# Performance work log

Measured on AMD Instinct MI355X. Metric: run time of the kernel, lower is better.

The kernel has to match this reference:

```python
import jax, jax.numpy as jnp
import numpy as np
import itertools, math

B, T, D = 4, 4096, 1024
H = 16
DIM = D // H          # 64
L, KB = 8, 4
R = 1 << KB           # 16
S = L * R             # 128
TOPK = 2


def setup_inputs() -> dict:
    key = jax.random.key(0)
    ks = jax.random.split(key, 8)
    x = jax.random.normal(ks[0], (B, T, D), dtype=jnp.float32)
    mask = jnp.ones((B, T), dtype=jnp.float32)
    sc = 1.0 / math.sqrt(D)
    Wq = jax.random.normal(ks[1], (D, D), dtype=jnp.float32) * sc
    Wk = jax.random.normal(ks[2], (D, D), dtype=jnp.float32) * sc
    Wv = jax.random.normal(ks[3], (D, D), dtype=jnp.float32) * sc
    Wout = jax.random.normal(ks[4], (D, D), dtype=jnp.float32) * sc
    b_out = jnp.zeros((D,), dtype=jnp.float32)
    # planes: (L, K_bits, head_dim) -> stored transposed as (head_dim, L*K_bits)
    planes = jax.random.normal(ks[5], (L * KB, DIM), dtype=jnp.float32)
    planes_T = planes.T
    # hypercube corners (R, K_bits) -> stored transposed as (K_bits, R)
    corners = jnp.asarray(list(itertools.product([-1.0, 1.0], repeat=KB)), dtype=jnp.float32)
    protos_T = corners.T
    logit_temp = jnp.zeros((), dtype=jnp.float32)  # log(1.0)
    return {"x": x, "mask": mask, "Wq": Wq, "Wk": Wk, "Wv": Wv,
            "Wout": Wout, "b_out": b_out, "planes_T": planes_T,
            "protos_T": protos_T, "logit_temp": logit_temp}


def reference(x, mask, Wq, Wk, Wv, Wout, b_out, planes_T, protos_T, logit_temp):
    b, t, d = x.shape
    Q = (x @ Wq).reshape(b, t, H, DIM)
    K = (x @ Wk).reshape(b, t, H, DIM)
    V = (x @ Wv).reshape(b, t, H, DIM)
    m = mask[:, :, None, None]
    Q, K, V = Q * m, K * m, V * m
    Q = jnp.transpose(Q, (0, 2, 1, 3))  # [B,H,T,dim]
    K = jnp.transpose(K, (0, 2, 1, 3))
    V = jnp.transpose(V, (0, 2, 1, 3))

    scale = jnp.clip(jnp.exp(logit_temp), 0.01, 20.0)
    # LSH hyperplane projections of K
    projK = jnp.einsum('bhtd,dp->bhtp', K, planes_T).reshape(b, H, t, L, KB)
    logitsK = jnp.einsum('bhtlk,kr->bhtlr', jnp.tanh(projK) / scale, protos_T)
    probsK = jax.nn.softmax(logitsK, axis=-1)  # [B,H,T,L,R]

    # top-k mask over R, then renormalize
    _, top_idx = jax.lax.top_k(probsK, TOPK)
    sel = jax.nn.one_hot(top_idx, R, dtype=probsK.dtype).sum(axis=-2)
    probsK = probsK * sel
    probsK = probsK / (probsK.sum(axis=-1, keepdims=True) + 1e-6)

    assign = probsK.reshape(b, H, t, S)  # [B,H,T,S]
    bucket_K = jnp.einsum('bhts,bhtd->bhsd', assign, K)
    bucket_V = jnp.einsum('bhts,bhtd->bhsd', assign, V)
    A = assign.sum(axis=2)[..., None]  # [B,H,S,1]
    bucket_K = bucket_K / (A + 1e-6)
    bucket_V = bucket_V / (A + 1e-6)

    scores = jnp.einsum('bhtd,bhsd->bhts', Q, bucket_K) / math.sqrt(DIM)
    probs_attn = jax.nn.softmax(scores, axis=-1)
    out = jnp.einsum('bhts,bhsd->bhtd', probs_attn, bucket_V)
    out = jnp.transpose(out, (0, 2, 1, 3)).reshape(b, t, d)
    return out @ Wout + b_out
```

## Files before the change

kernel.cpp:

```cpp
#include <hip/hip_runtime.h>
#include <math.h>
#include <stdint.h>

#define TT   4096
#define DD   1024
#define HH   16
#define DIMM 64
#define SS   128

typedef short bf16x8 __attribute__((ext_vector_type(8)));
typedef float f32x4  __attribute__((ext_vector_type(4)));

__device__ __forceinline__ unsigned short f2bf(float f) {
    uint32_t u = __float_as_uint(f);
    return (unsigned short)((u + 0x7fffu + ((u >> 16) & 1u)) >> 16);
}
__device__ __forceinline__ float bf2f(unsigned short h) {
    return __uint_as_float((uint32_t)h << 16);
}

#define GLD16(ldsp, gp) __builtin_amdgcn_global_load_lds( \
    (const __attribute__((address_space(1))) uint32_t*)(gp), \
    (__attribute__((address_space(3))) uint32_t*)(ldsp), 16, 0, 0)

__global__ __launch_bounds__(256) void cvt2_k(const float* __restrict__ x,
                                              unsigned short* __restrict__ xb,
                                              unsigned short* __restrict__ xlo)
{
    const size_t i = ((size_t)blockIdx.x * 256 + threadIdx.x) * 8;
    const float4 a = *(const float4*)&x[i];
    const float4 b = *(const float4*)&x[i + 4];
    const float v[8] = {a.x, a.y, a.z, a.w, b.x, b.y, b.z, b.w};
    unsigned short h[8], l[8];
#pragma unroll
    for (int j = 0; j < 8; j++) {
        h[j] = f2bf(v[j]);
        l[j] = f2bf(v[j] - bf2f(h[j]));
    }
    uint4 rh, rl;
    rh.x = (uint32_t)h[0] | ((uint32_t)h[1] << 16);
    rh.y = (uint32_t)h[2] | ((uint32_t)h[3] << 16);
    rh.z = (uint32_t)h[4] | ((uint32_t)h[5] << 16);
    rh.w = (uint32_t)h[6] | ((uint32_t)h[7] << 16);
    rl.x = (uint32_t)l[0] | ((uint32_t)l[1] << 16);
    rl.y = (uint32_t)l[2] | ((uint32_t)l[3] << 16);
    rl.z = (uint32_t)l[4] | ((uint32_t)l[5] << 16);
    rl.w = (uint32_t)l[6] | ((uint32_t)l[7] << 16);
    *(uint4*)&xb[i]  = rh;
    *(uint4*)&xlo[i] = rl;
}

__global__ __launch_bounds__(256) void tr_k(const float* __restrict__ W,
                                            unsigned short* __restrict__ WT)
{
    __shared__ unsigned short tile[32][33];
    const int bx = blockIdx.x * 32;
    const int by = blockIdx.y * 32;
    const int tx = threadIdx.x & 31, ty = threadIdx.x >> 5;
#pragma unroll
    for (int r = 0; r < 4; r++) {
        const int row = by + ty * 4 + r;
        tile[tx][ty * 4 + r] = f2bf(W[(size_t)row * 1024 + bx + tx]);
    }
    __syncthreads();
#pragma unroll
    for (int r = 0; r < 4; r++) {
        const int col = bx + ty * 4 + r;
        WT[(size_t)col * 1024 + by + tx] = tile[ty * 4 + r][tx];
    }
}

__global__ __launch_bounds__(256) void tr2_k(const float* __restrict__ Wp,
                                             unsigned short* __restrict__ WphT,
                                             unsigned short* __restrict__ WplT)
{
    __shared__ float tile[32][33];
    const int bx = blockIdx.x * 32;
    const int by = blockIdx.y * 32;
    const int tx = threadIdx.x & 31, ty = threadIdx.x >> 5;
#pragma unroll
    for (int r = 0; r < 4; r++) {
        const int row = by + ty * 4 + r;
        tile[tx][ty * 4 + r] = Wp[(size_t)row * 512 + bx + tx];
    }
    __syncthreads();
#pragma unroll
    for (int r = 0; r < 4; r++) {
        const int col = bx + ty * 4 + r;
        const float v = tile[ty * 4 + r][tx];
        const unsigned short hi = f2bf(v);
        const unsigned short lo = f2bf(v - bf2f(hi));
        WphT[(size_t)col * 1024 + by + tx] = hi;
        WplT[(size_t)col * 1024 + by + tx] = lo;
    }
}

__global__ __launch_bounds__(256) void qkv_k(
    const unsigned short* __restrict__ Abf, const unsigned short* __restrict__ BT,
    const float* __restrict__ mask, unsigned short* __restrict__ Qf,
    float* __restrict__ Kb, float* __restrict__ Vb)
{
    __shared__ short sA[2][4096];
    __shared__ short sB[2][4096];
    const int tid = threadIdx.x;
    const int w  = tid >> 6;
    const int ln = tid & 63;
    const int wm = w & 1, wn = w >> 1;
    const int id   = blockIdx.y * 24 + blockIdx.x;
    const int xcd  = id & 7, kk = id >> 3;
    const int band = xcd * 16 + kk / 24;
    const int colblk = kk % 24;
    const int row0 = band * 128;
    const int col0 = colblk * 128;
    const int lr = ln >> 4, lc = ln & 15;

    f32x4 acc[4][4];
#pragma unroll
    for (int i = 0; i < 4; i++)
#pragma unroll
        for (int j = 0; j < 4; j++) acc[i][j] = (f32x4){0.f, 0.f, 0.f, 0.f};

    const int ia0 = 2 * w, ia1 = 2 * w + 1;
    const size_t gA0 = (size_t)(row0 + ia0 * 16 + lc) * 1024 + lr * 8;
    const size_t gA1 = (size_t)(row0 + ia1 * 16 + lc) * 1024 + lr * 8;
    const size_t gB0 = (size_t)(col0 + ia0 * 16 + lc) * 1024 + lr * 8;
    const size_t gB1 = (size_t)(col0 + ia1 * 16 + lc) * 1024 + lr * 8;

    auto STAGE = [&](int buf, int k0) {
        GLD16(&sA[buf][ia0 * 512], Abf + gA0 + k0);
        GLD16(&sA[buf][ia1 * 512], Abf + gA1 + k0);
        GLD16(&sB[buf][ia0 * 512], BT  + gB0 + k0);
        GLD16(&sB[buf][ia1 * 512], BT  + gB1 + k0);
    };

    STAGE(0, 0);
    __syncthreads();
    for (int t = 0; t < 32; t++) {
        const int cur = t & 1;
        if (t < 31) STAGE(cur ^ 1, (t + 1) * 32);
        bf16x8 af[4], bfr[4];
#pragma unroll
        for (int ib = 0; ib < 4; ib++)
            af[ib] = *(const bf16x8*)&sA[cur][(wm * 4 + ib) * 512 + ln * 8];
#pragma unroll
        for (int jb = 0; jb < 4; jb++)
            bfr[jb] = *(const bf16x8*)&sB[cur][(wn * 4 + jb) * 512 + ln * 8];
#pragma unroll
        for (int ib = 0; ib < 4; ib++)
#pragma unroll
            for (int jb = 0; jb < 4; jb++)
                acc[ib][jb] = __builtin_amdgcn_mfma_f32_16x16x32_bf16(
                    af[ib], bfr[jb], acc[ib][jb], 0, 0, 0);
        __syncthreads();
    }

    const int proj = colblk >> 3;
    const int c0l  = (colblk & 7) * 128;
    const int h    = c0l / 64 + wn;
    if (proj == 0) {
#pragma unroll
        for (int ib = 0; ib < 4; ib++) {
#pragma unroll
            for (int r = 0; r < 4; r++) {
                const int gr = row0 + wm * 64 + ib * 16 + lr * 4 + r;
                const float mval = mask[gr];
                const int b = gr >> 12;
                const int tt = gr & 127;
                const size_t tbase = (size_t)(b * HH + h) * 262144
                                   + (size_t)((gr & (TT - 1)) >> 7) * 8192;
#pragma unroll
                for (int jb = 0; jb < 4; jb++) {
                    const int d = jb * 16 + lc;
                    const int e = ((tt >> 4) * 2 + (d >> 5)) * 512 +
                                  ((tt & 15) + ((d >> 3) & 3) * 16) * 8 + (d & 7);
                    Qf[tbase + e] = f2bf(acc[ib][jb][r] * mval);
                }
            }
        }
    } else {
        float* C = (proj == 1) ? Kb : Vb;
#pragma unroll
        for (int ib = 0; ib < 4; ib++) {
#pragma unroll
            for (int r = 0; r < 4; r++) {
                const int gr = row0 + wm * 64 + ib * 16 + lr * 4 + r;
                const float mval = mask[gr];
                const int b = gr >> 12, t = gr & (TT - 1);
                float* base = C + (((size_t)(b * HH + h) * TT + t) * DIMM);
#pragma unroll
                for (int jb = 0; jb < 4; jb++)
                    base[jb * 16 + lc] = acc[ib][jb][r] * mval;
            }
        }
    }
}

__global__ __launch_bounds__(256) void out_k(
    const unsigned short* __restrict__ Abf, const unsigned short* __restrict__ BT,
    const float* __restrict__ bias, float* __restrict__ C)
{
    __shared__ short sA[2][4096];
    __shared__ short sB[2][4096];
    const int tid = threadIdx.x;
    const int w  = tid >> 6, ln = tid & 63;
    const int wm = w & 1, wn = w >> 1;
    const int id  = blockIdx.y * 8 + blockIdx.x;
    const int xcd = id & 7, kk = id >> 3;
    const int row0 = (xcd * 16 + (kk >> 3)) * 128;
    const int col0 = (kk & 7) * 128;
    const int lr = ln >> 4, lc = ln & 15;

    f32x4 acc[4][4];
#pragma unroll
    for (int i = 0; i < 4; i++)
#pragma unroll
        for (int j = 0; j < 4; j++) acc[i][j] = (f32x4){0.f, 0.f, 0.f, 0.f};

    const int ia0 = 2 * w, ia1 = 2 * w + 1;
    const size_t gA0 = (size_t)(row0 + ia0 * 16 + lc) * 1024 + lr * 8;
    const size_t gA1 = (size_t)(row0 + ia1 * 16 + lc) * 1024 + lr * 8;
    const size_t gB0 = (size_t)(col0 + ia0 * 16 + lc) * 1024 + lr * 8;
    const size_t gB1 = (size_t)(col0 + ia1 * 16 + lc) * 1024 + lr * 8;

    auto STAGE = [&](int buf, int k0) {
        GLD16(&sA[buf][ia0 * 512], Abf + gA0 + k0);
        GLD16(&sA[buf][ia1 * 512], Abf + gA1 + k0);
        GLD16(&sB[buf][ia0 * 512], BT  + gB0 + k0);
        GLD16(&sB[buf][ia1 * 512], BT  + gB1 + k0);
    };

    STAGE(0, 0);
    __syncthreads();
    for (int t = 0; t < 32; t++) {
        const int cur = t & 1;
        if (t < 31) STAGE(cur ^ 1, (t + 1) * 32);
        bf16x8 af[4], bfr[4];
#pragma unroll
        for (int ib = 0; ib < 4; ib++)
            af[ib] = *(const bf16x8*)&sA[cur][(wm * 4 + ib) * 512 + ln * 8];
#pragma unroll
        for (int jb = 0; jb < 4; jb++)
            bfr[jb] = *(const bf16x8*)&sB[cur][(wn * 4 + jb) * 512 + ln * 8];
#pragma unroll
        for (int ib = 0; ib < 4; ib++)
#pragma unroll
            for (int jb = 0; jb < 4; jb++)
                acc[ib][jb] = __builtin_amdgcn_mfma_f32_16x16x32_bf16(
                    af[ib], bfr[jb], acc[ib][jb], 0, 0, 0);
        __syncthreads();
    }

#pragma unroll
    for (int ib = 0; ib < 4; ib++) {
#pragma unroll
        for (int r = 0; r < 4; r++) {
            const int gr = row0 + wm * 64 + ib * 16 + lr * 4 + r;
#pragma unroll
            for (int jb = 0; jb < 4; jb++) {
                const int col = col0 + wn * 64 + jb * 16 + lc;
                C[(size_t)gr * 1024 + col] = acc[ib][jb][r] + bias[col];
            }
        }
    }
}

__global__ __launch_bounds__(256) void projm_k(
    const unsigned short* __restrict__ Ah, const unsigned short* __restrict__ Al,
    const unsigned short* __restrict__ Bh, const unsigned short* __restrict__ Bl,
    const float* __restrict__ mask, float* __restrict__ P)
{
    __shared__ short sAh[2][4096];
    __shared__ short sAl[2][4096];
    __shared__ short sBh[2][4096];
    __shared__ short sBl[2][4096];
    const int tid = threadIdx.x;
    const int w  = tid >> 6;
    const int ln = tid & 63;
    const int wm = w & 1, wn = w >> 1;
    const int id  = blockIdx.y * 4 + blockIdx.x;
    const int xcd = id & 7, kk = id >> 3;
    const int row0 = (xcd * 16 + (kk >> 2)) * 128;
    const int col0 = (kk & 3) * 128;
    const int lr = ln >> 4, lc = ln & 15;

    f32x4 acc[4][4];
#pragma unroll
    for (int i = 0; i < 4; i++)
#pragma unroll
        for (int j = 0; j < 4; j++) acc[i][j] = (f32x4){0.f, 0.f, 0.f, 0.f};

    const int ia0 = 2 * w, ia1 = 2 * w + 1;
    const size_t gA0 = (size_t)(row0 + ia0 * 16 + lc) * 1024 + lr * 8;
    const size_t gA1 = (size_t)(row0 + ia1 * 16 + lc) * 1024 + lr * 8;
    const size_t gB0 = (size_t)(col0 + ia0 * 16 + lc) * 1024 + lr * 8;
    const size_t gB1 = (size_t)(col0 + ia1 * 16 + lc) * 1024 + lr * 8;

    auto STAGE = [&](int buf, int k0) {
        GLD16(&sAh[buf][ia0 * 512], Ah + gA0 + k0);
        GLD16(&sAh[buf][ia1 * 512], Ah + gA1 + k0);
        GLD16(&sAl[buf][ia0 * 512], Al + gA0 + k0);
        GLD16(&sAl[buf][ia1 * 512], Al + gA1 + k0);
        GLD16(&sBh[buf][ia0 * 512], Bh + gB0 + k0);
        GLD16(&sBh[buf][ia1 * 512], Bh + gB1 + k0);
        GLD16(&sBl[buf][ia0 * 512], Bl + gB0 + k0);
        GLD16(&sBl[buf][ia1 * 512], Bl + gB1 + k0);
    };

    STAGE(0, 0);
    __syncthreads();
    for (int t = 0; t < 32; t++) {
        const int cur = t & 1;
        if (t < 31) STAGE(cur ^ 1, (t + 1) * 32);
        bf16x8 ah[4], al[4], bh[4], bl[4];
#pragma unroll
        for (int ib = 0; ib < 4; ib++) {
            ah[ib] = *(const bf16x8*)&sAh[cur][(wm * 4 + ib) * 512 + ln * 8];
            al[ib] = *(const bf16x8*)&sAl[cur][(wm * 4 + ib) * 512 + ln * 8];
        }
#pragma unroll
        for (int jb = 0; jb < 4; jb++) {
            bh[jb] = *(const bf16x8*)&sBh[cur][(wn * 4 + jb) * 512 + ln * 8];
            bl[jb] = *(const bf16x8*)&sBl[cur][(wn * 4 + jb) * 512 + ln * 8];
        }
#pragma unroll
        for (int ib = 0; ib < 4; ib++)
#pragma unroll
            for (int jb = 0; jb < 4; jb++) {
                acc[ib][jb] = __builtin_amdgcn_mfma_f32_16x16x32_bf16(
                    ah[ib], bh[jb], acc[ib][jb], 0, 0, 0);
                acc[ib][jb] = __builtin_amdgcn_mfma_f32_16x16x32_bf16(
                    ah[ib], bl[jb], acc[ib][jb], 0, 0, 0);
                acc[ib][jb] = __builtin_amdgcn_mfma_f32_16x16x32_bf16(
                    al[ib], bh[jb], acc[ib][jb], 0, 0, 0);
            }
        __syncthreads();
    }

#pragma unroll
    for (int ib = 0; ib < 4; ib++) {
#pragma unroll
        for (int r = 0; r < 4; r++) {
            const int gr = row0 + wm * 64 + ib * 16 + lr * 4 + r;
            const float mval = mask[gr];
            const int b = gr >> 12, t = gr & (TT - 1);
#pragma unroll
            for (int jb = 0; jb < 4; jb++) {
                const int c = col0 + wn * 64 + jb * 16 + lc;
                const int h = c >> 5, p = c & 31;
                P[(((size_t)(b * HH + h) * TT + t) * 32) + p] =
                    acc[ib][jb][r] * mval;
            }
        }
    }
}

__global__ __launch_bounds__(256) void wproj_k(
    const float* __restrict__ Wk, const float* __restrict__ planesT,
    float* __restrict__ Wp)
{
    __shared__ float sW[1024];
    __shared__ float sP[2048];
    const int tid = threadIdx.x;
    const int k = blockIdx.x;
    for (int i = tid; i < 1024; i += 256) sW[i] = Wk[(size_t)k * 1024 + i];
    for (int i = tid; i < 2048; i += 256) sP[i] = planesT[i];
    __syncthreads();
#pragma unroll
    for (int c0 = 0; c0 < 2; c0++) {
        const int c = c0 * 256 + tid;
        const int h = c >> 5, p = c & 31;
        float s = 0.f;
#pragma unroll
        for (int d = 0; d < 64; d++)
            s = fmaf(sW[h * 64 + d], sP[d * 32 + p], s);
        Wp[(size_t)k * 512 + c] = s;
    }
}

__global__ __launch_bounds__(256) void zero_k(float* __restrict__ p)
{
    const size_t i = ((size_t)blockIdx.x * 256 + threadIdx.x) * 4;
    *(float4*)&p[i] = make_float4(0.f, 0.f, 0.f, 0.f);
}

__global__ __launch_bounds__(256) void assign_k(
    const float* __restrict__ Pj, const float* __restrict__ protosT,
    const float* __restrict__ logit_temp,
    unsigned char* __restrict__ aIdx, float* __restrict__ aW,
    float* __restrict__ gA)
{
    __shared__ float sPr[4][16];
    __shared__ float sCnt[SS];
    const int tid = threadIdx.x;
    const int tc = blockIdx.x;
    const int bh = blockIdx.y;

    if (tid < 64)  ((float*)sPr)[tid] = protosT[tid];
    if (tid < SS)  sCnt[tid] = 0.f;
    __syncthreads();

    const float scale = fminf(fmaxf(__expf(logit_temp[0]), 0.01f), 20.0f);
    const float inv_scale = 1.0f / scale;

    const int t = tc * 256 + tid;
    const float* pr = Pj + ((size_t)bh * TT + t) * 32;
    float proj[32];
#pragma unroll
    for (int j = 0; j < 8; j++) {
        const float4 v = *(const float4*)&pr[j * 4];
        proj[j * 4 + 0] = v.x; proj[j * 4 + 1] = v.y;
        proj[j * 4 + 2] = v.z; proj[j * 4 + 3] = v.w;
    }
#pragma unroll
    for (int p = 0; p < 32; p++) proj[p] = tanhf(proj[p]) * inv_scale;

    unsigned char idx[16];
    float wv[16];
#pragma unroll
    for (int l = 0; l < 8; l++) {
        float g[16];
#pragma unroll
        for (int r = 0; r < 16; r++)
            g[r] = proj[l * 4 + 0] * sPr[0][r] + proj[l * 4 + 1] * sPr[1][r] +
                   proj[l * 4 + 2] * sPr[2][r] + proj[l * 4 + 3] * sPr[3][r];
        float mx = g[0];
#pragma unroll
        for (int r = 1; r < 16; r++) mx = fmaxf(mx, g[r]);
        float Zs = 0.f;
#pragma unroll
        for (int r = 0; r < 16; r++) Zs += __expf(g[r] - mx);
        int a = 0; float ga = g[0];
#pragma unroll
        for (int r = 1; r < 16; r++) { if (g[r] > ga) { ga = g[r]; a = r; } }
        int b2 = (a == 0) ? 1 : 0; float gb = g[b2];
#pragma unroll
        for (int r = 0; r < 16; r++) { if (r != a && g[r] > gb) { gb = g[r]; b2 = r; } }
        const float pa = __expf(ga - mx) / Zs;
        const float pb = __expf(gb - mx) / Zs;
        const float den = pa + pb + 1e-6f;
        const float wa = pa / den, wb = pb / den;
        idx[l * 2 + 0] = (unsigned char)(l * 16 + a);  wv[l * 2 + 0] = wa;
        idx[l * 2 + 1] = (unsigned char)(l * 16 + b2); wv[l * 2 + 1] = wb;
        atomicAdd(&sCnt[l * 16 + a],  wa);
        atomicAdd(&sCnt[l * 16 + b2], wb);
    }
    const size_t off = (size_t)bh * TT + t;
    uint32_t pk[4];
#pragma unroll
    for (int j = 0; j < 4; j++)
        pk[j] = (uint32_t)idx[j * 4] | ((uint32_t)idx[j * 4 + 1] << 8) |
                ((uint32_t)idx[j * 4 + 2] << 16) | ((uint32_t)idx[j * 4 + 3] << 24);
    *(uint4*)&aIdx[off * 16] = make_uint4(pk[0], pk[1], pk[2], pk[3]);
#pragma unroll
    for (int j = 0; j < 4; j++)
        *(float4*)&aW[off * 16 + j * 4] =
            make_float4(wv[j * 4], wv[j * 4 + 1], wv[j * 4 + 2], wv[j * 4 + 3]);
    __syncthreads();
    if (tid < SS) atomicAdd(&gA[bh * SS + tid], sCnt[tid]);
}

__global__ __launch_bounds__(256) void scatter4_k(
    const float* __restrict__ Kb, const float* __restrict__ Vb,
    const unsigned char* __restrict__ aIdx, const float* __restrict__ aW,
    float* __restrict__ gBK, float* __restrict__ gBV)
{
    __shared__ short sA[8192];
    __shared__ short sB[8192];
    const int tid = threadIdx.x;
    const int tc = blockIdx.x;
    const int bh = blockIdx.y;
    const int w  = tid >> 6, ln = tid & 63;
    const int wm = w & 1, wn = w >> 1;

    f32x4 acc[4][4];
#pragma unroll
    for (int i = 0; i < 4; i++)
#pragma unroll
        for (int j = 0; j < 4; j++) acc[i][j] = (f32x4){0.f, 0.f, 0.f, 0.f};

    const int scol = tid & 127;
    const int stg  = tid >> 7;
    const float* srcrow = (scol < 64)
        ? Kb + (size_t)bh * (TT * DIMM) + scol
        : Vb + (size_t)bh * (TT * DIMM) + (scol - 64);
    const int bchunk = (scol >> 4);
    const int bslot8 = (scol & 15) * 8;
    const int ptt = tid >> 2, pg = tid & 3;

    for (int c = 0; c < 8; c++) {
        const int t0 = tc * 512 + c * 64;
        __syncthreads();
        {
            const uint4 z = make_uint4(0u, 0u, 0u, 0u);
#pragma unroll
            for (int r = 0; r < 4; r++)
                *(uint4*)&sA[(r * 256 + tid) * 8] = z;
        }
        __syncthreads();
#pragma unroll 8
        for (int r = 0; r < 32; r++) {
            const int tt = stg * 32 + r;
            const float v = srcrow[(size_t)(t0 + tt) * DIMM];
            sB[((tt >> 5) * 8 + bchunk) * 512 + ((tt >> 3) & 3) * 128 +
               bslot8 + (tt & 7)] = f2bf(v);
        }
        {
            const size_t off = (size_t)bh * TT + (t0 + ptt);
            const uint32_t pk = ((const uint32_t*)aIdx)[off * 4 + pg];
            const float4 wv = *(const float4*)&aW[off * 16 + pg * 4];
            const float w4[4] = {wv.x, wv.y, wv.z, wv.w};
#pragma unroll
            for (int q = 0; q < 4; q++) {
                const int s = (pk >> (8 * q)) & 255;
                sA[((ptt >> 5) * 8 + (s >> 4)) * 512 + ((ptt >> 3) & 3) * 128 +
                   (s & 15) * 8 + (ptt & 7)] = f2bf(w4[q]);
            }
        }
        __syncthreads();
#pragma unroll
        for (int ks = 0; ks < 2; ks++) {
            bf16x8 af[4], bfr[4];
#pragma unroll
            for (int ib = 0; ib < 4; ib++)
                af[ib] = *(const bf16x8*)&sA[(ks * 8 + wm * 4 + ib) * 512 + ln * 8];
#pragma unroll
            for (int jb = 0; jb < 4; jb++)
                bfr[jb] = *(const bf16x8*)&sB[(ks * 8 + wn * 4 + jb) * 512 + ln * 8];
#pragma unroll
            for (int ib = 0; ib < 4; ib++)
#pragma unroll
                for (int jb = 0; jb < 4; jb++)
                    acc[ib][jb] = __builtin_amdgcn_mfma_f32_16x16x32_bf16(
                        af[ib], bfr[jb], acc[ib][jb], 0, 0, 0);
        }
    }

    const int lr = ln >> 4, lc = ln & 15;
#pragma unroll
    for (int ib = 0; ib < 4; ib++) {
#pragma unroll
        for (int r = 0; r < 4; r++) {
            const int s = wm * 64 + ib * 16 + lr * 4 + r;
#pragma unroll
            for (int jb = 0; jb < 4; jb++) {
                const int col = wn * 64 + jb * 16 + lc;
                if (col < 64)
                    atomicAdd(&gBK[(size_t)bh * (SS * DIMM) + s * DIMM + col],
                              acc[ib][jb][r]);
                else
                    atomicAdd(&gBV[(size_t)bh * (SS * DIMM) + s * DIMM + (col - 64)],
                              acc[ib][jb][r]);
            }
        }
    }
}

__global__ __launch_bounds__(256) void bprep_k(
    const float* __restrict__ gBK, const float* __restrict__ gBV,
    const float* __restrict__ gA,
    unsigned short* __restrict__ Kf, unsigned short* __restrict__ VTf)
{
    __shared__ float sInv[SS];
    const int tid = threadIdx.x;
    const int bh = blockIdx.y;
    if (tid < SS) sInv[tid] = 1.0f / (gA[bh * SS + tid] + 1e-6f);
    __syncthreads();
#pragma unroll
    for (int it = 0; it < 8; it++) {
        const int i = (blockIdx.x * 8 + it) * 256 + tid;
        const int s = i >> 6, d = i & 63;
        const float kv = gBK[(size_t)bh * 8192 + i] * sInv[s];
        const float vv = gBV[(size_t)bh * 8192 + i] * sInv[s];
        const int ek = ((s >> 4) * 2 + (d >> 5)) * 512 +
                       ((s & 15) + ((d >> 3) & 3) * 16) * 8 + (d & 7);
        const int ev = ((d >> 4) * 4 + (s >> 5)) * 512 +
                       ((d & 15) + ((s >> 3) & 3) * 16) * 8 + (s & 7);
        Kf[(size_t)bh * 8192 + ek]  = f2bf(kv);
        VTf[(size_t)bh * 8192 + ev] = f2bf(vv);
    }
}

__global__ __launch_bounds__(256) void attn_m(
    const unsigned short* __restrict__ Qf, const unsigned short* __restrict__ Kf,
    const unsigned short* __restrict__ VTf, unsigned short* __restrict__ attb)
{
    __shared__ short sQ[8192];
    __shared__ short sK[8192];
    __shared__ short sVT[8192];
    __shared__ short sP[16384];
    const int tid = threadIdx.x;
    const int tc = blockIdx.x;
    const int bh = blockIdx.y;
    const int w = tid >> 6, l = tid & 63;

    const size_t qbase  = (size_t)bh * 262144 + (size_t)tc * 8192;
    const size_t kvbase = (size_t)bh * 8192;
#pragma unroll
    for (int i = 0; i < 4; i++) {
        const int o = (i * 256 + w * 64) * 8;
        GLD16(&sQ[o],  Qf  + qbase  + o + l * 8);
        GLD16(&sK[o],  Kf  + kvbase + o + l * 8);
        GLD16(&sVT[o], VTf + kvbase + o + l * 8);
    }
    __syncthreads();

    f32x4 acc[2][8];
#pragma unroll
    for (int i = 0; i < 2; i++)
#pragma unroll
        for (int j = 0; j < 8; j++) acc[i][j] = (f32x4){0.f, 0.f, 0.f, 0.f};

#pragma unroll
    for (int ks = 0; ks < 2; ks++) {
        const bf16x8 a0 = *(const bf16x8*)&sQ[((w * 2 + 0) * 2 + ks) * 512 + l * 8];
        const bf16x8 a1 = *(const bf16x8*)&sQ[((w * 2 + 1) * 2 + ks) * 512 + l * 8];
#pragma unroll
        for (int jb = 0; jb < 8; jb++) {
            const bf16x8 b = *(const bf16x8*)&sK[(jb * 2 + ks) * 512 + l * 8];
            acc[0][jb] = __builtin_amdgcn_mfma_f32_16x16x32_bf16(a0, b, acc[0][jb], 0, 0, 0);
            acc[1][jb] = __builtin_amdgcn_mfma_f32_16x16x32_bf16(a1, b, acc[1][jb], 0, 0, 0);
        }
    }

#pragma unroll
    for (int ib = 0; ib < 2; ib++) {
        const int mb = w * 2 + ib;
#pragma unroll
        for (int r = 0; r < 4; r++) {
            float v[8];
            float mx = -INFINITY;
#pragma unroll
            for (int jb = 0; jb < 8; jb++) {
                v[jb] = acc[ib][jb][r] * 0.125f;
                mx = fmaxf(mx, v[jb]);
            }
            mx = fmaxf(mx, __shfl_xor(mx, 1));
            mx = fmaxf(mx, __shfl_xor(mx, 2));
            mx = fmaxf(mx, __shfl_xor(mx, 4));
            mx = fmaxf(mx, __shfl_xor(mx, 8));
            float Z = 0.f;
#pragma unroll
            for (int jb = 0; jb < 8; jb++) { v[jb] = __expf(v[jb] - mx); Z += v[jb]; }
            Z += __shfl_xor(Z, 1);
            Z += __shfl_xor(Z, 2);
            Z += __shfl_xor(Z, 4);
            Z += __shfl_xor(Z, 8);
            const float invZ = 1.0f / Z;
            const int ttl = (l >> 4) * 4 + r;
#pragma unroll
            for (int jb = 0; jb < 8; jb++) {
                int e = (mb * 4 + (jb >> 1)) * 512 +
                        (ttl + (((jb * 2 + ((l >> 3) & 1)) & 3) * 16)) * 8 + (l & 7);
                e ^= ((e >> 7) & 3) << 4;
                sP[e] = (short)f2bf(v[jb] * invZ);
            }
        }
    }

    f32x4 acc2[2][4];
#pragma unroll
    for (int i = 0; i < 2; i++)
#pragma unroll
        for (int j = 0; j < 4; j++) acc2[i][j] = (f32x4){0.f, 0.f, 0.f, 0.f};

#pragma unroll
    for (int ks = 0; ks < 4; ks++) {
        bf16x8 a[2];
#pragma unroll
        for (int ib = 0; ib < 2; ib++) {
            int ia = ((w * 2 + ib) * 4 + ks) * 512 + l * 8;
            ia ^= ((ia >> 7) & 3) << 4;
            a[ib] = *(const bf16x8*)&sP[ia];
        }
#pragma unroll
        for (int jb = 0; jb < 4; jb++) {
            const bf16x8 b = *(const bf16x8*)&sVT[(jb * 4 + ks) * 512 + l * 8];
            acc2[0][jb] = __builtin_amdgcn_mfma_f32_16x16x32_bf16(a[0], b, acc2[0][jb], 0, 0, 0);
            acc2[1][jb] = __builtin_amdgcn_mfma_f32_16x16x32_bf16(a[1], b, acc2[1][jb], 0, 0, 0);
        }
    }

    const int b = bh >> 4, h = bh & 15;
#pragma unroll
    for (int ib = 0; ib < 2; ib++) {
#pragma unroll
        for (int r = 0; r < 4; r++) {
            const int t = tc * 128 + w * 32 + ib * 16 + (l >> 4) * 4 + r;
            unsigned short* outp = attb + ((size_t)(b * TT + t)) * DD + h * DIMM;
#pragma unroll
            for (int jb = 0; jb < 4; jb++)
                outp[jb * 16 + (l & 15)] = f2bf(acc2[ib][jb][r]);
        }
    }
}

extern "C" void kernel_launch(void* const* d_in, const int* in_sizes, int n_in,
                              void* d_out, int out_size, void* d_ws, size_t ws_size,
                              hipStream_t stream)
{
    const float* x       = (const float*)d_in[0];
    const float* mask    = (const float*)d_in[1];
    const float* Wq      = (const float*)d_in[2];
    const float* Wk      = (const float*)d_in[3];
    const float* Wv      = (const float*)d_in[4];
    const float* Wout    = (const float*)d_in[5];
    const float* b_out   = (const float*)d_in[6];
    const float* planesT = (const float*)d_in[7];
    const float* protosT = (const float*)d_in[8];
    const float* ltemp   = (const float*)d_in[9];
    float* out = (float*)d_out;

    float* ws  = (float*)d_ws;
    float* Kb  = ws + (1u << 24);
    float* Vb  = ws + (2u << 24);
    float* gBK = ws + (3u << 24);
    float* gBV = gBK + 524288;
    float* gA  = gBV + 524288;
    unsigned short* Qf    = (unsigned short*)ws;
    unsigned short* xb    = (unsigned short*)(ws + 51388416);
    unsigned short* xlo   = (unsigned short*)Vb;
    float*          Wp    = ws;
    unsigned short* WphT  = (unsigned short*)(ws + 524288);
    unsigned short* WplT  = (unsigned short*)(ws + 786432);
    float*          aW    = ws + 51388416;
    unsigned char*  aIdx  = (unsigned char*)(ws + 55582720);
    unsigned short* Kf    = (unsigned short*)(ws + 56631296);
    unsigned short* VTf   = (unsigned short*)(ws + 56893440);
    unsigned short* attb  = (unsigned short*)Vb;
    unsigned short* WoutT = (unsigned short*)(ws + 41943040);
    float*          Pj    = (float*)d_out;
    unsigned short* BTall = (unsigned short*)((float*)d_out + 8388608);

    const dim3 tg(32, 32);
    const dim3 t2g(16, 32);
    const dim3 pg(4, 128);
    const dim3 qg(24, 128);
    const dim3 og(8, 128);

    cvt2_k<<<8192, 256, 0, stream>>>(x, xb, xlo);

    wproj_k<<<1024, 256, 0, stream>>>(Wk, planesT, Wp);
    tr2_k<<<t2g, 256, 0, stream>>>(Wp, WphT, WplT);
    projm_k<<<pg, 256, 0, stream>>>(xb, xlo, WphT, WplT, mask, Pj);

    tr_k<<<tg, 256, 0, stream>>>(Wq, BTall);
    tr_k<<<tg, 256, 0, stream>>>(Wk, BTall + 1048576);
    tr_k<<<tg, 256, 0, stream>>>(Wv, BTall + 2097152);
    qkv_k<<<qg, 256, 0, stream>>>(xb, BTall, mask, Qf, Kb, Vb);

    zero_k<<<1032, 256, 0, stream>>>(gBK);
    assign_k<<<dim3(16, 64), 256, 0, stream>>>(Pj, protosT, ltemp, aIdx, aW, gA);
    scatter4_k<<<dim3(8, 64), 256, 0, stream>>>(Kb, Vb, aIdx, aW, gBK, gBV);

    bprep_k<<<dim3(4, 64), 256, 0, stream>>>(gBK, gBV, gA, Kf, VTf);
    tr_k<<<tg, 256, 0, stream>>>(Wout, WoutT);
    attn_m<<<dim3(32, 64), 256, 0, stream>>>(Qf, Kf, VTf, attb);

    out_k<<<og, 256, 0, stream>>>(attb, WoutT, b_out, out);
}
```

Before: 659.9 us.

## Write K/V as bf16 MFMA-ready tiles via LDS-staged epilogue, load directly in scatter

After: 629.9 us. -4.5%, faster.

```diff
diff --git a/kernel.cpp b/kernel.cpp
--- a/kernel.cpp
+++ b/kernel.cpp
@@ -98,18 +98,20 @@
 __global__ __launch_bounds__(256) void qkv_k(
     const unsigned short* __restrict__ Abf, const unsigned short* __restrict__ BT,
     const float* __restrict__ mask, unsigned short* __restrict__ Qf,
-    float* __restrict__ Kb, float* __restrict__ Vb)
-{
-    __shared__ short sA[2][4096];
-    __shared__ short sB[2][4096];
+    unsigned short* __restrict__ KVf)
+{
+    __shared__ short sMem[16384];
+    short* sA = sMem;
+    short* sB = sMem + 8192;
     const int tid = threadIdx.x;
     const int w  = tid >> 6;
     const int ln = tid & 63;
     const int wm = w & 1, wn = w >> 1;
     const int id   = blockIdx.y * 24 + blockIdx.x;
     const int xcd  = id & 7, kk = id >> 3;
-    const int band = xcd * 16 + kk / 24;
-    const int colblk = kk % 24;
+    const int cg   = kk / 192, rem = kk % 192;
+    const int band = xcd * 16 + rem / 12;
+    const int colblk = cg * 12 + rem % 12;
     const int row0 = band * 128;
     const int col0 = colblk * 128;
     const int lr = ln >> 4, lc = ln & 15;
@@ -127,10 +129,10 @@
     const size_t gB1 = (size_t)(col0 + ia1 * 16 + lc) * 1024 + lr * 8;
 
     auto STAGE = [&](int buf, int k0) {
-        GLD16(&sA[buf][ia0 * 512], Abf + gA0 + k0);
-        GLD16(&sA[buf][ia1 * 512], Abf + gA1 + k0);
-        GLD16(&sB[buf][ia0 * 512], BT  + gB0 + k0);
-        GLD16(&sB[buf][ia1 * 512], BT  + gB1 + k0);
+        GLD16(&sA[buf * 4096 + ia0 * 512], Abf + gA0 + k0);
+        GLD16(&sA[buf * 4096 + ia1 * 512], Abf + gA1 + k0);
+        GLD16(&sB[buf * 4096 + ia0 * 512], BT  + gB0 + k0);
+        GLD16(&sB[buf * 4096 + ia1 * 512], BT  + gB1 + k0);
     };
 
     STAGE(0, 0);
@@ -141,10 +143,10 @@
         bf16x8 af[4], bfr[4];
 #pragma unroll
         for (int ib = 0; ib < 4; ib++)
-            af[ib] = *(const bf16x8*)&sA[cur][(wm * 4 + ib) * 512 + ln * 8];
+            af[ib] = *(const bf16x8*)&sA[cur * 4096 + (wm * 4 + ib) * 512 + ln * 8];
 #pragma unroll
         for (int jb = 0; jb < 4; jb++)
-            bfr[jb] = *(const bf16x8*)&sB[cur][(wn * 4 + jb) * 512 + ln * 8];
+            bfr[jb] = *(const bf16x8*)&sB[cur * 4096 + (wn * 4 + jb) * 512 + ln * 8];
 #pragma unroll
         for (int ib = 0; ib < 4; ib++)
 #pragma unroll
@@ -155,42 +157,68 @@
     }
 
     const int proj = colblk >> 3;
-    const int c0l  = (colblk & 7) * 128;
-    const int h    = c0l / 64 + wn;
+    const int b    = row0 >> 12;
+    const int h0   = (colblk & 7) * 2;
+    short* sT = sMem;
+
     if (proj == 0) {
 #pragma unroll
         for (int ib = 0; ib < 4; ib++) {
 #pragma unroll
             for (int r = 0; r < 4; r++) {
-                const int gr = row0 + wm * 64 + ib * 16 + lr * 4 + r;
-                const float mval = mask[gr];
-                const int b = gr >> 12;
-                const int tt = gr & 127;
-                const size_t tbase = (size_t)(b * HH + h) * 262144
-                                   + (size_t)((gr & (TT - 1)) >> 7) * 8192;
+                const int tt = wm * 64 + ib * 16 + lr * 4 + r;
+                const float mval = mask[row0 + tt];
 #pragma unroll
                 for (int jb = 0; jb < 4; jb++) {
                     const int d = jb * 16 + lc;
                     const int e = ((tt >> 4) * 2 + (d >> 5)) * 512 +
                                   ((tt & 15) + ((d >> 3) & 3) * 16) * 8 + (d & 7);
-                    Qf[tbase + e] = f2bf(acc[ib][jb][r] * mval);
+                    sT[wn * 8192 + e] = (short)f2bf(acc[ib][jb][r] * mval);
                 }
             }
         }
+        __syncthreads();
+        const int tile = (row0 & (TT - 1)) >> 7;
+#pragma unroll
+        for (int i = 0; i < 8; i++) {
+            const int flat = i * 256 + tid;
+            const int h_l  = flat >> 10;
+            const int off  = (flat & 1023) * 8;
+            unsigned short* dst = Qf + (size_t)(b * HH + h0 + h_l) * 262144
+                                + (size_t)tile * 8192 + off;
+            *(uint4*)dst = *(const uint4*)&sT[h_l * 8192 + off];
+        }
     } else {
-        float* C = (proj == 1) ? Kb : Vb;
+        const int voff = (proj == 2) ? 4 : 0;
 #pragma unroll
         for (int ib = 0; ib < 4; ib++) {
 #pragma unroll
             for (int r = 0; r < 4; r++) {
-                const int gr = row0 + wm * 64 + ib * 16 + lr * 4 + r;
-                const float mval = mask[gr];
-                const int b = gr >> 12, t = gr & (TT - 1);
-                float* base = C + (((size_t)(b * HH + h) * TT + t) * DIMM);
+                const int tt128 = wm * 64 + ib * 16 + lr * 4 + r;
+                const float mval = mask[row0 + tt128];
+                const int chunk = tt128 >> 6, tt6 = tt128 & 63;
+                const int rbase = (wn * 2 + chunk) * 4096 +
+                                  ((tt6 >> 3) & 3) * 128 + lc * 8 + (tt6 & 7);
+                const int t5 = (tt6 >> 5) * 4 * 512;
 #pragma unroll
                 for (int jb = 0; jb < 4; jb++)
-                    base[jb * 16 + lc] = acc[ib][jb][r] * mval;
-            }
+                    sT[rbase + t5 + jb * 512] = (short)f2bf(acc[ib][jb][r] * mval);
+            }
+        }
+        __syncthreads();
+        const int gc0 = (row0 & (TT - 1)) >> 6;
+#pragma unroll
+        for (int i = 0; i < 8; i++) {
+            const int flat = i * 256 + tid;
+            const int bf = flat >> 6;
+            const int wi = flat & 63;
+            const int h_l = bf >> 4, chunk = (bf >> 3) & 1;
+            const int tt5 = (bf >> 2) & 1, nb = bf & 3;
+            const int lidx = (h_l * 2 + chunk) * 4096 + (tt5 * 4 + nb) * 512 + wi * 8;
+            const size_t gidx = (size_t)(b * HH + h0 + h_l) * 524288
+                              + (size_t)(gc0 + chunk) * 8192
+                              + (size_t)(tt5 * 8 + nb + voff) * 512 + wi * 8;
+            *(uint4*)&KVf[gidx] = *(const uint4*)&sT[lidx];
         }
     }
 }
@@ -460,7 +488,7 @@
 }
 
 __global__ __launch_bounds__(256) void scatter4_k(
-    const float* __restrict__ Kb, const float* __restrict__ Vb,
+    const unsigned short* __restrict__ KVf,
     const unsigned char* __restrict__ aIdx, const float* __restrict__ aW,
     float* __restrict__ gBK, float* __restrict__ gBV)
 {
@@ -478,33 +506,26 @@
 #pragma unroll
         for (int j = 0; j < 4; j++) acc[i][j] = (f32x4){0.f, 0.f, 0.f, 0.f};
 
-    const int scol = tid & 127;
-    const int stg  = tid >> 7;
-    const float* srcrow = (scol < 64)
-        ? Kb + (size_t)bh * (TT * DIMM) + scol
-        : Vb + (size_t)bh * (TT * DIMM) + (scol - 64);
-    const int bchunk = (scol >> 4);
-    const int bslot8 = (scol & 15) * 8;
+    const size_t kvbase = (size_t)bh * 524288;
     const int ptt = tid >> 2, pg = tid & 3;
 
     for (int c = 0; c < 8; c++) {
-        const int t0 = tc * 512 + c * 64;
+        __syncthreads();
+        const size_t cbase = kvbase + (size_t)(tc * 8 + c) * 8192;
+#pragma unroll
+        for (int i = 0; i < 4; i++) {
+            const int seg = w * 4 + i;
+            GLD16(&sB[seg * 512], KVf + cbase + seg * 512 + ln * 8);
+        }
+        {
+            const uint4 z = make_uint4(0u, 0u, 0u, 0u);
+#pragma unroll
+            for (int r = 0; r < 4; r++)
+                *(uint4*)&sA[(r * 256 + tid) * 8] = z;
+        }
         __syncthreads();
         {
-            const uint4 z = make_uint4(0u, 0u, 0u, 0u);
-#pragma unroll
-            for (int r = 0; r < 4; r++)
-                *(uint4*)&sA[(r * 256 + tid) * 8] = z;
-        }
-        __syncthreads();
-#pragma unroll 8
-        for (int r = 0; r < 32; r++) {
-            const int tt = stg * 32 + r;
-            const float v = srcrow[(size_t)(t0 + tt) * DIMM];
-            sB[((tt >> 5) * 8 + bchunk) * 512 + ((tt >> 3) & 3) * 128 +
-               bslot8 + (tt & 7)] = f2bf(v);
-        }
-        {
+            const int t0 = tc * 512 + c * 64;
             const size_t off = (size_t)bh * TT + (t0 + ptt);
             const uint32_t pk = ((const uint32_t*)aIdx)[off * 4 + pg];
             const float4 wv = *(const float4*)&aW[off * 16 + pg * 4];
@@ -711,14 +732,14 @@
     float* out = (float*)d_out;
 
     float* ws  = (float*)d_ws;
-    float* Kb  = ws + (1u << 24);
-    float* Vb  = ws + (2u << 24);
     float* gBK = ws + (3u << 24);
     float* gBV = gBK + 524288;
     float* gA  = gBV + 524288;
     unsigned short* Qf    = (unsigned short*)ws;
+    unsigned short* BTall = (unsigned short*)(ws + (1u << 24));
+    unsigned short* KVf   = (unsigned short*)(ws + (2u << 24));
+    unsigned short* xlo   = KVf;
     unsigned short* xb    = (unsigned short*)(ws + 51388416);
-    unsigned short* xlo   = (unsigned short*)Vb;
     float*          Wp    = ws;
     unsigned short* WphT  = (unsigned short*)(ws + 524288);
     unsigned short* WplT  = (unsigned short*)(ws + 786432);
@@ -726,10 +747,9 @@
     unsigned char*  aIdx  = (unsigned char*)(ws + 55582720);
     unsigned short* Kf    = (unsigned short*)(ws + 56631296);
     unsigned short* VTf   = (unsigned short*)(ws + 56893440);
-    unsigned short* attb  = (unsigned short*)Vb;
+    unsigned short* attb  = KVf;
     unsigned short* WoutT = (unsigned short*)(ws + 41943040);
     float*          Pj    = (float*)d_out;
-    unsigned short* BTall = (unsigned short*)((float*)d_out + 8388608);
 
     const dim3 tg(32, 32);
     const dim3 t2g(16, 32);
@@ -746,11 +766,11 @@
     tr_k<<<tg, 256, 0, stream>>>(Wq, BTall);
     tr_k<<<tg, 256, 0, stream>>>(Wk, BTall + 1048576);
     tr_k<<<tg, 256, 0, stream>>>(Wv, BTall + 2097152);
-    qkv_k<<<qg, 256, 0, stream>>>(xb, BTall, mask, Qf, Kb, Vb);
+    qkv_k<<<qg, 256, 0, stream>>>(xb, BTall, mask, Qf, KVf);
 
     zero_k<<<1032, 256, 0, stream>>>(gBK);
     assign_k<<<dim3(16, 64), 256, 0, stream>>>(Pj, protosT, ltemp, aIdx, aW, gA);
-    scatter4_k<<<dim3(8, 64), 256, 0, stream>>>(Kb, Vb, aIdx, aW, gBK, gBV);
+    scatter4_k<<<dim3(8, 64), 256, 0, stream>>>(KVf, aIdx, aW, gBK, gBV);
 
     bprep_k<<<dim3(4, 64), 256, 0, stream>>>(gBK, gBV, gA, Kf, VTf);
     tr_k<<<tg, 256, 0, stream>>>(Wout, WoutT);
```
